# Kernel tuning notes

Hardware: AMD Instinct MI355X
Metric: run time of the kernel (lower is better)

## Reference

```python
import jax, jax.numpy as jnp
import numpy as np

STATE_DIM = 32
CONTROL_DIM = 8
EMBED_DIM = 96
LATENT_DIM = STATE_DIM + EMBED_DIM  # 128
HIDDEN = 512
B, M = 2048, 64


def setup_inputs() -> dict:
    key = jax.random.key(0)
    ks = jax.random.split(key, 16)
    s = lambda k, shp, fan: jax.random.normal(k, shp, jnp.float32) * (1.0 / np.sqrt(fan))
    return {
        "x_k": jax.random.normal(ks[0], (B, STATE_DIM), jnp.float32),
        "u_seq": jax.random.normal(ks[1], (B, M, CONTROL_DIM), jnp.float32),
        "x_next_seq": jax.random.normal(ks[2], (B, M, STATE_DIM), jnp.float32),
        # encoder MLP (depth=3): in->h, h->h, h->h, h->embed
        "W1": s(ks[3], (STATE_DIM, HIDDEN), STATE_DIM), "b1": jnp.zeros((HIDDEN,), jnp.float32),
        "W2": s(ks[4], (HIDDEN, HIDDEN), HIDDEN), "b2": jnp.zeros((HIDDEN,), jnp.float32),
        "W3": s(ks[5], (HIDDEN, HIDDEN), HIDDEN), "b3": jnp.zeros((HIDDEN,), jnp.float32),
        "Wo": s(ks[6], (HIDDEN, EMBED_DIM), HIDDEN), "bo": jnp.zeros((EMBED_DIM,), jnp.float32),
        # Koopman operators (Linear, no bias); stored as [in, out]
        "A": s(ks[7], (LATENT_DIM, LATENT_DIM), LATENT_DIM),
        "Bmat": s(ks[8], (CONTROL_DIM, LATENT_DIM), CONTROL_DIM),
    }


def _encode(x, W1, b1, W2, b2, W3, b3, Wo, bo):
    h = jax.nn.relu(x @ W1 + b1)
    h = jax.nn.relu(h @ W2 + b2)
    h = jax.nn.relu(h @ W3 + b3)
    return h @ Wo + bo


def _lift(x, W1, b1, W2, b2, W3, b3, Wo, bo):
    return jnp.concatenate([x, _encode(x, W1, b1, W2, b2, W3, b3, Wo, bo)], axis=-1)


def reference(x_k, u_seq, x_next_seq, W1, b1, W2, b2, W3, b3, Wo, bo, A, Bmat):
    m = u_seq.shape[1]
    z_k = _lift(x_k, W1, b1, W2, b2, W3, b3, Wo, bo)  # [B, L]
    # lift targets (encoder applied to flattened [B*M, S])
    z_target_seq = _lift(x_next_seq.reshape(-1, STATE_DIM), W1, b1, W2, b2, W3, b3, Wo, bo)
    z_target_seq = z_target_seq.reshape(-1, m, LATENT_DIM)
    # precompute control contributions, then sequential LTI recurrence via scan
    bu = jnp.einsum('bmc,cl->mbl', u_seq, Bmat)  # [M, B, L]

    def step(z, bu_i):
        z_next = z @ A + bu_i
        return z_next, z_next

    _, z_pred = jax.lax.scan(step, z_k, bu)  # [M, B, L]
    z_pred_seq = jnp.transpose(z_pred, (1, 0, 2))  # [B, M, L]
    x_pred_seq = z_pred_seq[..., :STATE_DIM]
    return (z_pred_seq, x_pred_seq, z_target_seq)
```

## Files before the change

kernel.cpp:

```cpp
#include <hip/hip_runtime.h>


typedef unsigned short u16;
typedef __attribute__((ext_vector_type(8))) short bf16x8;
typedef __attribute__((ext_vector_type(4))) short bf16x4;
typedef __attribute__((ext_vector_type(4))) float f32x4;

#define OFF_W1 0
#define OFF_W2 16384
#define OFF_W3 278528
#define OFF_WO 540672
#define OFF_ZK_BYTES 1179648
#define OFF_AH 1114112
#define OFF_AL 1130496

#define XPRED_OFF 16777216
#define ZTGT_OFF  20971520

__device__ __forceinline__ float bf2f(u16 u) {
  unsigned int i = ((unsigned int)u) << 16;
  return __builtin_bit_cast(float, i);
}
__device__ __forceinline__ u16 f2bf(float f) {
  unsigned int i = __builtin_bit_cast(unsigned int, f);
  i = (i + 0x7FFFu + ((i >> 16) & 1u)) >> 16;
  return (u16)i;
}

__global__ void prep_swizzle(const float* __restrict__ W1, const float* __restrict__ W2,
                             const float* __restrict__ W3, const float* __restrict__ Wo,
                             const float* __restrict__ Am, u16* __restrict__ dst) {
  int f = blockIdx.x;
  int l = threadIdx.x;
  const float* src; int K, N; u16* d; int lo = 0;
  if (f < 32)        { src = W1; K = 32;  N = 512; d = dst + OFF_W1; }
  else if (f < 544)  { src = W2; K = 512; N = 512; d = dst + OFF_W2; f -= 32; }
  else if (f < 1056) { src = W3; K = 512; N = 512; d = dst + OFF_W3; f -= 544; }
  else if (f < 1152) { src = Wo; K = 512; N = 96;  d = dst + OFF_WO; f -= 1056; }
  else if (f < 1184) { src = Am; K = 128; N = 128; d = dst + OFF_AH; f -= 1152; }
  else               { src = Am; K = 128; N = 128; d = dst + OFF_AL; f -= 1184; lo = 1; }
  const int KF = K >> 5;
  const int ct = f / KF, ks = f - ct * KF;
  const int q = l >> 4, n = l & 15;
  const int kbase = ks * 32 + q * 8;
  const int col = ct * 16 + n;
  bf16x8 vh;
  #pragma unroll
  for (int j = 0; j < 8; ++j) {
    float v = src[(size_t)(kbase + j) * N + col];
    u16 h = f2bf(v);
    if (lo) h = f2bf(v - bf2f(h));
    vh[j] = (short)h;
  }
  *(bf16x8*)(d + ((size_t)f * 64 + l) * 8) = vh;
}

__device__ __forceinline__ void store_h(const f32x4 (&acc)[4][8],
                                        const float* __restrict__ bias,
                                        u16* hbuf, int rh, int cg, int q, int n) {
  __syncthreads();
  #pragma unroll
  for (int i = 0; i < 8; ++i) {
    const int col = cg * 128 + i * 16 + n;
    const float bia = bias[col];
    #pragma unroll
    for (int rg = 0; rg < 4; ++rg) {
      const int rb = rh * 64 + rg * 16 + q * 4;
      float f0 = fmaxf(acc[rg][i][0] + bia, 0.f);
      float f1 = fmaxf(acc[rg][i][1] + bia, 0.f);
      float f2 = fmaxf(acc[rg][i][2] + bia, 0.f);
      float f3 = fmaxf(acc[rg][i][3] + bia, 0.f);
      unsigned p01, p23;
      asm("v_cvt_pk_bf16_f32 %0, %1, %2" : "=v"(p01) : "v"(f0), "v"(f1));
      asm("v_cvt_pk_bf16_f32 %0, %1, %2" : "=v"(p23) : "v"(f2), "v"(f3));
      hbuf[((rb + 0) * 512 + col) ^ (((rb + 0) & 7) << 3)] = (u16)(p01 & 0xFFFFu);
      hbuf[((rb + 1) * 512 + col) ^ (((rb + 1) & 7) << 3)] = (u16)(p01 >> 16);
      hbuf[((rb + 2) * 512 + col) ^ (((rb + 2) & 7) << 3)] = (u16)(p23 & 0xFFFFu);
      hbuf[((rb + 3) * 512 + col) ^ (((rb + 3) & 7) << 3)] = (u16)(p23 >> 16);
    }
  }
  __syncthreads();
}

__device__ __forceinline__ void big_layer(const u16* __restrict__ wb,
                                          const float* __restrict__ bias,
                                          u16* hbuf, int rh, int cg, int l, int q, int n) {
  f32x4 acc[4][8];
  #pragma unroll
  for (int rg = 0; rg < 4; ++rg)
    #pragma unroll
    for (int i = 0; i < 8; ++i) acc[rg][i] = (f32x4){0.f, 0.f, 0.f, 0.f};
  #pragma unroll 2
  for (int ks = 0; ks < 16; ++ks) {
    bf16x8 b[8], a[4];
    #pragma unroll
    for (int i = 0; i < 8; ++i)
      b[i] = *(const bf16x8*)(wb + (size_t)((8 * cg + i) * 16 + ks) * 512 + (size_t)l * 8);
    #pragma unroll
    for (int rg = 0; rg < 4; ++rg) {
      const int row = rh * 64 + rg * 16 + n;
      a[rg] = *(const bf16x8*)&hbuf[(row * 512 + ks * 32 + q * 8) ^ ((row & 7) << 3)];
    }
    #pragma unroll
    for (int rg = 0; rg < 4; ++rg)
      #pragma unroll
      for (int i = 0; i < 8; ++i)
        acc[rg][i] = __builtin_amdgcn_mfma_f32_16x16x32_bf16(a[rg], b[i], acc[rg][i], 0, 0, 0);
  }
  store_h(acc, bias, hbuf, rh, cg, q, n);
}

__global__ __launch_bounds__(512, 2) void encoder_tgt(
    const float* __restrict__ xnext, const u16* __restrict__ wf,
    const float* __restrict__ b1, const float* __restrict__ b2,
    const float* __restrict__ b3, const float* __restrict__ bo_,
    float* __restrict__ ztgt) {
  __shared__ __align__(16) u16 hbuf[128 * 512];
  const int tid = threadIdx.x;
  const int wv = tid >> 6, l = tid & 63;
  const int q = l >> 4, n = l & 15;
  const int rh = wv >> 2, cg = wv & 3;
  const size_t row0 = (size_t)blockIdx.x * 128;

  {
    const int r = tid >> 2, k0 = (tid & 3) * 8;
    f32x4 x0 = *(const f32x4*)(xnext + (row0 + r) * 32 + k0);
    f32x4 x1 = *(const f32x4*)(xnext + (row0 + r) * 32 + k0 + 4);
    *(f32x4*)(ztgt + (row0 + r) * 128 + k0)     = x0;
    *(f32x4*)(ztgt + (row0 + r) * 128 + k0 + 4) = x1;
    bf16x8 v;
    #pragma unroll
    for (int j = 0; j < 4; ++j) { v[j] = (short)f2bf(x0[j]); v[4 + j] = (short)f2bf(x1[j]); }
    *(bf16x8*)&hbuf[(r * 512 + k0) ^ ((r & 7) << 3)] = v;
  }
  __syncthreads();

  {
    f32x4 acc[4][8];
    #pragma unroll
    for (int rg = 0; rg < 4; ++rg)
      #pragma unroll
      for (int i = 0; i < 8; ++i) acc[rg][i] = (f32x4){0.f, 0.f, 0.f, 0.f};
    bf16x8 a[4];
    #pragma unroll
    for (int rg = 0; rg < 4; ++rg) {
      const int row = rh * 64 + rg * 16 + n;
      a[rg] = *(const bf16x8*)&hbuf[(row * 512 + q * 8) ^ ((row & 7) << 3)];
    }
    #pragma unroll
    for (int i = 0; i < 8; ++i) {
      bf16x8 b = *(const bf16x8*)(wf + OFF_W1 + (size_t)(8 * cg + i) * 512 + (size_t)l * 8);
      #pragma unroll
      for (int rg = 0; rg < 4; ++rg)
        acc[rg][i] = __builtin_amdgcn_mfma_f32_16x16x32_bf16(a[rg], b, acc[rg][i], 0, 0, 0);
    }
    store_h(acc, b1, hbuf, rh, cg, q, n);
  }

  big_layer(wf + OFF_W2, b2, hbuf, rh, cg, l, q, n);
  big_layer(wf + OFF_W3, b3, hbuf, rh, cg, l, q, n);

  if (wv < 6) {
    f32x4 o[8];
    #pragma unroll
    for (int rg = 0; rg < 8; ++rg) o[rg] = (f32x4){0.f, 0.f, 0.f, 0.f};
    #pragma unroll 2
    for (int ks = 0; ks < 16; ++ks) {
      bf16x8 b = *(const bf16x8*)(wf + OFF_WO + (size_t)(wv * 16 + ks) * 512 + (size_t)l * 8);
      #pragma unroll
      for (int rg = 0; rg < 8; ++rg) {
        const int row = rg * 16 + n;
        bf16x8 a = *(const bf16x8*)&hbuf[(row * 512 + ks * 32 + q * 8) ^ ((row & 7) << 3)];
        o[rg] = __builtin_amdgcn_mfma_f32_16x16x32_bf16(a, b, o[rg], 0, 0, 0);
      }
    }
    const float bia = bo_[wv * 16 + n];
    #pragma unroll
    for (int rg = 0; rg < 8; ++rg)
      #pragma unroll
      for (int r = 0; r < 4; ++r)
        ztgt[(row0 + rg * 16 + q * 4 + r) * 128 + 32 + wv * 16 + n] = o[rg][r] + bia;
  }
}

__global__ __launch_bounds__(512) void encoder_zk_f32(
    const float* __restrict__ xk,
    const float* __restrict__ W1, const float* __restrict__ b1,
    const float* __restrict__ W2, const float* __restrict__ b2,
    const float* __restrict__ W3, const float* __restrict__ b3,
    const float* __restrict__ Wo, const float* __restrict__ bo_,
    float* __restrict__ zk_out) {
  __shared__ __align__(16) float hb[2][8][512];
  __shared__ __align__(16) float xb[8][32];
  const int t = threadIdx.x;
  const int row0 = blockIdx.x * 8;
  if (t < 256) {
    int r = t >> 5, j = t & 31;
    float v = xk[(size_t)(row0 + r) * 32 + j];
    xb[r][j] = v;
    zk_out[(size_t)(row0 + r) * 128 + j] = v;
  }
  __syncthreads();
  const int c = t;
  {
    float a[8];
    const float i0 = b1[c];
    #pragma unroll
    for (int r = 0; r < 8; ++r) a[r] = i0;
    for (int k = 0; k < 32; k += 4) {
      float w0 = W1[(size_t)(k+0)*512 + c];
      float w1 = W1[(size_t)(k+1)*512 + c];
      float w2 = W1[(size_t)(k+2)*512 + c];
      float w3 = W1[(size_t)(k+3)*512 + c];
      #pragma unroll
      for (int r = 0; r < 8; ++r) {
        f32x4 z = *(const f32x4*)&xb[r][k];
        a[r] += z[0]*w0 + z[1]*w1 + z[2]*w2 + z[3]*w3;
      }
    }
    #pragma unroll
    for (int r = 0; r < 8; ++r) hb[0][r][c] = fmaxf(a[r], 0.f);
  }
  __syncthreads();
  #pragma unroll
  for (int lyr = 0; lyr < 2; ++lyr) {
    const float* W = lyr ? W3 : W2;
    const float* bb = lyr ? b3 : b2;
    const float (*hin)[512] = hb[lyr & 1];
    float (*hout)[512] = hb[(lyr & 1) ^ 1];
    float a[8];
    const float i0 = bb[c];
    #pragma unroll
    for (int r = 0; r < 8; ++r) a[r] = i0;
    for (int k = 0; k < 512; k += 4) {
      float w0 = W[(size_t)(k+0)*512 + c];
      float w1 = W[(size_t)(k+1)*512 + c];
      float w2 = W[(size_t)(k+2)*512 + c];
      float w3 = W[(size_t)(k+3)*512 + c];
      #pragma unroll
      for (int r = 0; r < 8; ++r) {
        f32x4 z = *(const f32x4*)&hin[r][k];
        a[r] += z[0]*w0 + z[1]*w1 + z[2]*w2 + z[3]*w3;
      }
    }
    #pragma unroll
    for (int r = 0; r < 8; ++r) hout[r][c] = fmaxf(a[r], 0.f);
    __syncthreads();
  }
  if (t < 96) {
    float a[8];
    const float i0 = bo_[t];
    #pragma unroll
    for (int r = 0; r < 8; ++r) a[r] = i0;
    for (int k = 0; k < 512; k += 4) {
      float w0 = Wo[(size_t)(k+0)*96 + t];
      float w1 = Wo[(size_t)(k+1)*96 + t];
      float w2 = Wo[(size_t)(k+2)*96 + t];
      float w3 = Wo[(size_t)(k+3)*96 + t];
      #pragma unroll
      for (int r = 0; r < 8; ++r) {
        f32x4 z = *(const f32x4*)&hb[0][r][k];
        a[r] += z[0]*w0 + z[1]*w1 + z[2]*w2 + z[3]*w3;
      }
    }
    #pragma unroll
    for (int r = 0; r < 8; ++r)
      zk_out[(size_t)(row0 + r) * 128 + 32 + t] = a[r];
  }
}

__global__ __launch_bounds__(512) void scan_mfma(
    const float* __restrict__ zk, const u16* __restrict__ wf,
    const float* __restrict__ Bm, const float* __restrict__ useq,
    float* __restrict__ zpred, float* __restrict__ xpred) {
  __shared__ __align__(16) u16 ahf[32 * 512];
  __shared__ __align__(16) u16 alf[32 * 512];
  __shared__ __align__(16) float ubuf[8 * 512];
  __shared__ __align__(16) float zbuf[8][132];
  __shared__ __align__(16) u16 zh[16][136];
  __shared__ __align__(16) u16 zl[16][136];
  __shared__ __align__(16) float bu[8][132];
  const int t = threadIdx.x;
  const int wv = t >> 6, l = t & 63;
  const int q = l >> 4, n = l & 15;
  const size_t b0 = (size_t)blockIdx.x * 8;

  #pragma unroll
  for (int i = 0; i < 4; ++i) {
    const int f = wv * 4 + i;
    __builtin_amdgcn_global_load_lds(
        (const __attribute__((address_space(1))) unsigned int*)(wf + OFF_AH + (size_t)f * 512 + l * 8),
        (__attribute__((address_space(3))) unsigned int*)(ahf + (size_t)f * 512), 16, 0, 0);
    __builtin_amdgcn_global_load_lds(
        (const __attribute__((address_space(1))) unsigned int*)(wf + OFF_AL + (size_t)f * 512 + l * 8),
        (__attribute__((address_space(3))) unsigned int*)(alf + (size_t)f * 512), 16, 0, 0);
  }
  {
    const float* us = useq + b0 * 512;
    *(f32x4*)&ubuf[t * 8]     = *(const f32x4*)(us + t * 8);
    *(f32x4*)&ubuf[t * 8 + 4] = *(const f32x4*)(us + t * 8 + 4);
  }
  if (t < 256) {
    const int r = t >> 5, c4 = (t & 31) * 4;
    *(f32x4*)&zbuf[r][c4] = *(const f32x4*)(zk + (b0 + r) * 128 + c4);
  }
  for (int i = t; i < 8 * 136; i += 512) { (&zh[8][0])[i] = 0; (&zl[8][0])[i] = 0; }
  float bm0[8], bm1[8];
  #pragma unroll
  for (int j = 0; j < 8; ++j) {
    bm0[j] = Bm[(size_t)j * 128 + 2 * l];
    bm1[j] = Bm[(size_t)j * 128 + 2 * l + 1];
  }
  __syncthreads();

  for (int s = 0; s < 64; ++s) {
    {
      float z0 = zbuf[wv][2 * l], z1 = zbuf[wv][2 * l + 1];
      u16 h0 = f2bf(z0), h1 = f2bf(z1);
      u16 lo0 = f2bf(z0 - bf2f(h0)), lo1 = f2bf(z1 - bf2f(h1));
      *(unsigned int*)&zh[wv][2 * l] = (unsigned int)h0 | ((unsigned int)h1 << 16);
      *(unsigned int*)&zl[wv][2 * l] = (unsigned int)lo0 | ((unsigned int)lo1 << 16);
      f32x4 ua = *(const f32x4*)&ubuf[wv * 512 + s * 8];
      f32x4 ub = *(const f32x4*)&ubuf[wv * 512 + s * 8 + 4];
      float bv0 = ua[0]*bm0[0] + ua[1]*bm0[1] + ua[2]*bm0[2] + ua[3]*bm0[3]
                + ub[0]*bm0[4] + ub[1]*bm0[5] + ub[2]*bm0[6] + ub[3]*bm0[7];
      float bv1 = ua[0]*bm1[0] + ua[1]*bm1[1] + ua[2]*bm1[2] + ua[3]*bm1[3]
                + ub[0]*bm1[4] + ub[1]*bm1[5] + ub[2]*bm1[6] + ub[3]*bm1[7];
      bu[wv][2 * l]     = bv0;
      bu[wv][2 * l + 1] = bv1;
    }
    __syncthreads();
    f32x4 aH = {0.f, 0.f, 0.f, 0.f};
    f32x4 aL = {0.f, 0.f, 0.f, 0.f};
    f32x4 aM = {0.f, 0.f, 0.f, 0.f};
    #pragma unroll
    for (int ks = 0; ks < 4; ++ks) {
      const int ko = ks * 32 + q * 8;
      bf16x8 azh = *(const bf16x8*)&zh[n][ko];
      bf16x8 azl = *(const bf16x8*)&zl[n][ko];
      bf16x8 bh = *(const bf16x8*)&ahf[(size_t)(wv * 4 + ks) * 512 + l * 8];
      bf16x8 bl = *(const bf16x8*)&alf[(size_t)(wv * 4 + ks) * 512 + l * 8];
      aH = __builtin_amdgcn_mfma_f32_16x16x32_bf16(azh, bh, aH, 0, 0, 0);
      aL = __builtin_amdgcn_mfma_f32_16x16x32_bf16(azl, bh, aL, 0, 0, 0);
      aM = __builtin_amdgcn_mfma_f32_16x16x32_bf16(azh, bl, aM, 0, 0, 0);
    }
    f32x4 acc = aH + aL;
    acc = acc + aM;
    if (q < 2) {
      #pragma unroll
      for (int r = 0; r < 4; ++r) {
        const int row = q * 4 + r;
        const int c = wv * 16 + n;
        const float v = acc[r] + bu[row][c];
        zbuf[row][c] = v;
        const size_t go = (b0 + row) * 64 + s;
        zpred[go * 128 + c] = v;
        if (wv < 2) xpred[go * 32 + c] = v;
      }
    }
    __syncthreads();
  }
}

extern "C" void kernel_launch(void* const* d_in, const int* in_sizes, int n_in,
                              void* d_out, int out_size, void* d_ws, size_t ws_size,
                              hipStream_t stream) {
  (void)in_sizes; (void)n_in; (void)out_size; (void)ws_size;
  const float* xk    = (const float*)d_in[0];
  const float* useq  = (const float*)d_in[1];
  const float* xnext = (const float*)d_in[2];
  const float* W1 = (const float*)d_in[3];
  const float* b1 = (const float*)d_in[4];
  const float* W2 = (const float*)d_in[5];
  const float* b2 = (const float*)d_in[6];
  const float* W3 = (const float*)d_in[7];
  const float* b3 = (const float*)d_in[8];
  const float* Wo = (const float*)d_in[9];
  const float* bo = (const float*)d_in[10];
  const float* A  = (const float*)d_in[11];
  const float* Bm = (const float*)d_in[12];

  float* out   = (float*)d_out;
  float* zpred = out;
  float* xpred = out + XPRED_OFF;
  float* ztgt  = out + ZTGT_OFF;
  u16*   wf    = (u16*)d_ws;
  float* zkw   = (float*)((char*)d_ws + OFF_ZK_BYTES);

  prep_swizzle<<<1216, 64, 0, stream>>>(W1, W2, W3, Wo, A, wf);
  encoder_zk_f32<<<256, 512, 0, stream>>>(xk, W1, b1, W2, b2, W3, b3, Wo, bo, zkw);
  scan_mfma<<<256, 512, 0, stream>>>(zkw, wf, Bm, useq, zpred, xpred);
  encoder_tgt<<<1024, 512, 0, stream>>>(xnext, wf, b1, b2, b3, bo, ztgt);
}
```

Before: 522.5 us.

## Double-buffer scan state in bf16 split form, one barrier per step

The scan kernel now keeps the recurrent state directly as hi/lo bf16 halves in double-buffered shared arrays. Each step's output writes the next buffer instead of going through an fp32 zbuf that was re-split at the start of the next step. The control term B·u is computed in registers, for the lanes that use it, one step ahead, which removes the bu buffer and one of the two __syncthreads per step. The encoder's occupancy hint changes from a launch_bounds minimum to amdgpu_waves_per_eu(2,2), which may alter register allocation there.

Measured after the change: 528.4 us. Within noise of the previous version (+1.1%).

```diff
diff --git a/kernel.cpp b/kernel.cpp
--- a/kernel.cpp
+++ b/kernel.cpp
@@ -110,7 +110,9 @@
   store_h(acc, bias, hbuf, rh, cg, q, n);
 }
 
-__global__ __launch_bounds__(512, 2) void encoder_tgt(
+__global__ __launch_bounds__(512)
+__attribute__((amdgpu_waves_per_eu(2, 2)))
+void encoder_tgt(
     const float* __restrict__ xnext, const u16* __restrict__ wf,
     const float* __restrict__ b1, const float* __restrict__ b2,
     const float* __restrict__ b3, const float* __restrict__ bo_,
@@ -276,10 +278,8 @@
   __shared__ __align__(16) u16 ahf[32 * 512];
   __shared__ __align__(16) u16 alf[32 * 512];
   __shared__ __align__(16) float ubuf[8 * 512];
-  __shared__ __align__(16) float zbuf[8][132];
-  __shared__ __align__(16) u16 zh[16][136];
-  __shared__ __align__(16) u16 zl[16][136];
-  __shared__ __align__(16) float bu[8][132];
+  __shared__ __align__(16) u16 zh[2][16][136];
+  __shared__ __align__(16) u16 zl[2][16][136];
   const int t = threadIdx.x;
   const int wv = t >> 6, l = t & 63;
   const int q = l >> 4, n = l & 15;
@@ -300,44 +300,46 @@
     *(f32x4*)&ubuf[t * 8]     = *(const f32x4*)(us + t * 8);
     *(f32x4*)&ubuf[t * 8 + 4] = *(const f32x4*)(us + t * 8 + 4);
   }
+  for (int i = t; i < 8 * 136; i += 512) {
+    (&zh[0][8][0])[i] = 0; (&zh[1][8][0])[i] = 0;
+    (&zl[0][8][0])[i] = 0; (&zl[1][8][0])[i] = 0;
+  }
   if (t < 256) {
     const int r = t >> 5, c4 = (t & 31) * 4;
-    *(f32x4*)&zbuf[r][c4] = *(const f32x4*)(zk + (b0 + r) * 128 + c4);
-  }
-  for (int i = t; i < 8 * 136; i += 512) { (&zh[8][0])[i] = 0; (&zl[8][0])[i] = 0; }
-  float bm0[8], bm1[8];
-  #pragma unroll
-  for (int j = 0; j < 8; ++j) {
-    bm0[j] = Bm[(size_t)j * 128 + 2 * l];
-    bm1[j] = Bm[(size_t)j * 128 + 2 * l + 1];
-  }
-  __syncthreads();
-
+    f32x4 z = *(const f32x4*)(zk + (b0 + r) * 128 + c4);
+    #pragma unroll
+    for (int i = 0; i < 4; ++i) {
+      u16 h = f2bf(z[i]);
+      zh[0][r][c4 + i] = h;
+      zl[0][r][c4 + i] = f2bf(z[i] - bf2f(h));
+    }
+  }
+  const int myc = wv * 16 + n;
+  float bmv[8];
+  #pragma unroll
+  for (int j = 0; j < 8; ++j) bmv[j] = Bm[(size_t)j * 128 + myc];
+  __syncthreads();
+
+  float bunow[4];
+  #pragma unroll
+  for (int r = 0; r < 4; ++r) {
+    const int row = (q & 1) * 4 + r;
+    f32x4 ua = *(const f32x4*)&ubuf[row * 512];
+    f32x4 ub = *(const f32x4*)&ubuf[row * 512 + 4];
+    bunow[r] = ua[0]*bmv[0] + ua[1]*bmv[1] + ua[2]*bmv[2] + ua[3]*bmv[3]
+             + ub[0]*bmv[4] + ub[1]*bmv[5] + ub[2]*bmv[6] + ub[3]*bmv[7];
+  }
+
+  int cur = 0;
   for (int s = 0; s < 64; ++s) {
-    {
-      float z0 = zbuf[wv][2 * l], z1 = zbuf[wv][2 * l + 1];
-      u16 h0 = f2bf(z0), h1 = f2bf(z1);
-      u16 lo0 = f2bf(z0 - bf2f(h0)), lo1 = f2bf(z1 - bf2f(h1));
-      *(unsigned int*)&zh[wv][2 * l] = (unsigned int)h0 | ((unsigned int)h1 << 16);
-      *(unsigned int*)&zl[wv][2 * l] = (unsigned int)lo0 | ((unsigned int)lo1 << 16);
-      f32x4 ua = *(const f32x4*)&ubuf[wv * 512 + s * 8];
-      f32x4 ub = *(const f32x4*)&ubuf[wv * 512 + s * 8 + 4];
-      float bv0 = ua[0]*bm0[0] + ua[1]*bm0[1] + ua[2]*bm0[2] + ua[3]*bm0[3]
-                + ub[0]*bm0[4] + ub[1]*bm0[5] + ub[2]*bm0[6] + ub[3]*bm0[7];
-      float bv1 = ua[0]*bm1[0] + ua[1]*bm1[1] + ua[2]*bm1[2] + ua[3]*bm1[3]
-                + ub[0]*bm1[4] + ub[1]*bm1[5] + ub[2]*bm1[6] + ub[3]*bm1[7];
-      bu[wv][2 * l]     = bv0;
-      bu[wv][2 * l + 1] = bv1;
-    }
-    __syncthreads();
     f32x4 aH = {0.f, 0.f, 0.f, 0.f};
     f32x4 aL = {0.f, 0.f, 0.f, 0.f};
     f32x4 aM = {0.f, 0.f, 0.f, 0.f};
     #pragma unroll
     for (int ks = 0; ks < 4; ++ks) {
       const int ko = ks * 32 + q * 8;
-      bf16x8 azh = *(const bf16x8*)&zh[n][ko];
-      bf16x8 azl = *(const bf16x8*)&zl[n][ko];
+      bf16x8 azh = *(const bf16x8*)&zh[cur][n][ko];
+      bf16x8 azl = *(const bf16x8*)&zl[cur][n][ko];
       bf16x8 bh = *(const bf16x8*)&ahf[(size_t)(wv * 4 + ks) * 512 + l * 8];
       bf16x8 bl = *(const bf16x8*)&alf[(size_t)(wv * 4 + ks) * 512 + l * 8];
       aH = __builtin_amdgcn_mfma_f32_16x16x32_bf16(azh, bh, aH, 0, 0, 0);
@@ -350,15 +352,27 @@
       #pragma unroll
       for (int r = 0; r < 4; ++r) {
         const int row = q * 4 + r;
-        const int c = wv * 16 + n;
-        const float v = acc[r] + bu[row][c];
-        zbuf[row][c] = v;
+        const float v = acc[r] + bunow[r];
+        u16 h = f2bf(v);
+        zh[cur ^ 1][row][myc] = h;
+        zl[cur ^ 1][row][myc] = f2bf(v - bf2f(h));
         const size_t go = (b0 + row) * 64 + s;
-        zpred[go * 128 + c] = v;
-        if (wv < 2) xpred[go * 32 + c] = v;
+        zpred[go * 128 + myc] = v;
+        if (wv < 2) xpred[go * 32 + myc] = v;
+      }
+    }
+    if (s < 63) {
+      #pragma unroll
+      for (int r = 0; r < 4; ++r) {
+        const int row = (q & 1) * 4 + r;
+        f32x4 ua = *(const f32x4*)&ubuf[row * 512 + (s + 1) * 8];
+        f32x4 ub = *(const f32x4*)&ubuf[row * 512 + (s + 1) * 8 + 4];
+        bunow[r] = ua[0]*bmv[0] + ua[1]*bmv[1] + ua[2]*bmv[2] + ua[3]*bmv[3]
+                 + ub[0]*bmv[4] + ub[1]*bmv[5] + ub[2]*bmv[6] + ub[3]*bmv[7];
       }
     }
     __syncthreads();
+    cur ^= 1;
   }
 }
 
```
